# Performance work log

Measured on AMD Instinct MI355X. Metric: run time of the kernel, lower is better.

Reference implementation:

```python
import jax, jax.numpy as jnp
import numpy as np

D_MODEL = 64
SEQ_LEN = 9
MAX_SL = 50
TIMESTAMP = 56
ACTION_NUM = 300
BATCH = 65536


def setup_inputs() -> dict:
    key = jax.random.key(0)
    ks = jax.random.split(key, 8)
    input_actions = jax.random.randint(ks[0], (BATCH, SEQ_LEN), 0, ACTION_NUM + 1)
    emb_table = jax.random.normal(ks[1], (ACTION_NUM + 1, D_MODEL), jnp.float32) * 0.02
    emb_table = emb_table.at[0].set(0.0)  # padding_idx=0
    M_w = jax.random.normal(ks[2], (MAX_SL, D_MODEL, D_MODEL), jnp.float32) * 0.05
    M_b = jax.random.normal(ks[3], (MAX_SL, D_MODEL), jnp.float32) * 0.05
    W_w = jax.random.normal(ks[4], (TIMESTAMP, D_MODEL, D_MODEL), jnp.float32) * 0.05
    W_b = jax.random.normal(ks[5], (TIMESTAMP, D_MODEL), jnp.float32) * 0.05
    out_w = jax.random.normal(ks[6], (ACTION_NUM, D_MODEL), jnp.float32) * 0.05
    out_b = jax.random.normal(ks[7], (ACTION_NUM,), jnp.float32) * 0.05
    return {"input_actions": input_actions, "emb_table": emb_table,
            "M_w": M_w, "M_b": M_b, "W_w": W_w, "W_b": W_b,
            "out_w": out_w, "out_b": out_b}


def reference(input_actions, emb_table, M_w, M_b, W_w, W_b, out_w, out_b):
    B, S = input_actions.shape
    d = emb_table.shape[1]
    ae = emb_table[input_actions]              # [B, S, d]
    ae_t = jnp.transpose(ae, (1, 0, 2))        # [S, B, d]
    # per-timestep weight selection, matching M[min(i, len(M)-1)] and W[i % timeStamp]
    m_idx = jnp.minimum(jnp.arange(S), M_w.shape[0] - 1)
    w_idx = jnp.arange(S) % W_w.shape[0]
    Mw, Mb = M_w[m_idx], M_b[m_idx]            # [S, d, d], [S, d]
    Ww, Wb = W_w[w_idx], W_b[w_idx]

    def step(hl, xs):
        x, mw, mb, ww, wb = xs
        # torch Linear: y = x @ W.T + b
        hl = jax.nn.sigmoid(x @ mw.T + mb + hl @ ww.T + wb)
        return hl, None

    hl0 = jnp.zeros((B, d), ae.dtype)
    hl, _ = jax.lax.scan(step, hl0, (ae_t, Mw, Mb, Ww, Wb))
    return hl @ out_w.T + out_b               # [B, actionNum]
```

## Files before the change

### kernel.cpp

```cpp
#include <hip/hip_runtime.h>
#include <hip/hip_bf16.h>


#define BATCH   65536
#define SEQ     9
#define DMODEL  64
#define ANUM    300
#define BT      64
#define LSTR    72

#define WS_M    0
#define WS_W    36864
#define WS_OW   73728
#define WS_EMB  94208
#define WS_END  113472
#define WS_BSUM_BYTES (WS_END * 2)

typedef __attribute__((ext_vector_type(8))) short  bf16x8;
typedef __attribute__((ext_vector_type(4))) float  f32x4;

__device__ __forceinline__ unsigned short f2b(float f) {
    union { float f; unsigned int u; } x; x.f = f;
    unsigned int r = x.u + 0x7FFFu + ((x.u >> 16) & 1u);
    return (unsigned short)(r >> 16);
}

#define PP_TOTAL (36864 + 20480 + 19264 + 576)

__global__ void prepack(const float* __restrict__ Mw, const float* __restrict__ Ww,
                        const float* __restrict__ outw, const float* __restrict__ emb,
                        const float* __restrict__ Mb, const float* __restrict__ Wb,
                        unsigned short* __restrict__ wsb, float* __restrict__ bsum)
{
    int t = blockIdx.x * 256 + threadIdx.x;
    if (t < 36864) {
        int j    = t & 7;
        int lane = (t >> 3) & 63;
        int kb   = (t >> 9) & 1;
        int nt   = (t >> 10) & 3;
        int s    = t >> 12;
        int nr   = nt * 16 + (lane & 15);
        int k    = kb * 32 + ((lane >> 4) << 3) + j;
        wsb[WS_M + t] = f2b(Mw[(s * DMODEL + nr) * DMODEL + k]);
        wsb[WS_W + t] = f2b(Ww[(s * DMODEL + nr) * DMODEL + k]);
        return;
    }
    t -= 36864;
    if (t < 20480) {
        int j    = t & 7;
        int lane = (t >> 3) & 63;
        int kb   = (t >> 9) & 1;
        int nt   = (t >> 10) & 3;
        int cc   = t >> 12;
        int col  = cc * 64 + nt * 16 + (lane & 15);
        int k    = kb * 32 + ((lane >> 4) << 3) + j;
        float v  = (col < ANUM) ? outw[col * DMODEL + k] : 0.f;
        wsb[WS_OW + t] = f2b(v);
        return;
    }
    t -= 20480;
    if (t < 19264) {
        wsb[WS_EMB + t] = f2b(emb[t]);
        return;
    }
    t -= 19264;
    if (t < 576) {
        bsum[t] = Mb[t] + Wb[t];
    }
}

__global__ __launch_bounds__(256, 4)
void carnn_main(const int* __restrict__ acts,
                const unsigned short* __restrict__ wsb,
                const float* __restrict__ bsum,
                const float* __restrict__ outb,
                float* __restrict__ out)
{
    __shared__ unsigned short Hl[BT * LSTR];

    const int tid  = threadIdx.x;
    const int lane = tid & 63;
    const int wv   = tid >> 6;
    const int lrow = lane & 15;
    const int quad = lane >> 4;
    const int m0   = wv * 16;

    const int brow = blockIdx.x * BT + m0 + lrow;
    const int row9 = brow * SEQ;

    for (int i = lane; i < 16 * LSTR; i += 64) Hl[m0 * LSTR + i] = 0;

    const unsigned short* Mp = wsb + WS_M;
    const unsigned short* Wp = wsb + WS_W;
    const unsigned short* Op = wsb + WS_OW;
    const unsigned short* Eb = wsb + WS_EMB;

    for (int s = 0; s < SEQ; ++s) {
        int id = acts[row9 + s];
        const bf16x8* ex = (const bf16x8*)(Eb + id * DMODEL);
        bf16x8 ax0 = ex[quad];
        bf16x8 ax1 = ex[4 + quad];
        bf16x8 ah0 = *(const bf16x8*)&Hl[(m0 + lrow) * LSTR + quad * 8];
        bf16x8 ah1 = *(const bf16x8*)&Hl[(m0 + lrow) * LSTR + 32 + quad * 8];

        #pragma unroll
        for (int nt = 0; nt < 4; ++nt) {
            const int fo = (s * 4 + nt) * 1024 + lane * 8;
            bf16x8 bm0 = *(const bf16x8*)&Mp[fo];
            bf16x8 bm1 = *(const bf16x8*)&Mp[fo + 512];
            bf16x8 bw0 = *(const bf16x8*)&Wp[fo];
            bf16x8 bw1 = *(const bf16x8*)&Wp[fo + 512];
            f32x4 acc = {0.f, 0.f, 0.f, 0.f};
            acc = __builtin_amdgcn_mfma_f32_16x16x32_bf16(ax0, bm0, acc, 0, 0, 0);
            acc = __builtin_amdgcn_mfma_f32_16x16x32_bf16(ax1, bm1, acc, 0, 0, 0);
            acc = __builtin_amdgcn_mfma_f32_16x16x32_bf16(ah0, bw0, acc, 0, 0, 0);
            acc = __builtin_amdgcn_mfma_f32_16x16x32_bf16(ah1, bw1, acc, 0, 0, 0);

            const int col  = nt * 16 + lrow;
            const float bias = bsum[s * DMODEL + col];
            #pragma unroll
            for (int r = 0; r < 4; ++r) {
                float v = acc[r] + bias;
                float h = 1.f / (1.f + __expf(-v));
                Hl[(m0 + quad * 4 + r) * LSTR + col] = f2b(h);
            }
        }
    }

    bf16x8 ah0 = *(const bf16x8*)&Hl[(m0 + lrow) * LSTR + quad * 8];
    bf16x8 ah1 = *(const bf16x8*)&Hl[(m0 + lrow) * LSTR + 32 + quad * 8];
    const int rowb = blockIdx.x * BT + m0 + quad * 4;

    #pragma unroll
    for (int cc = 0; cc < 5; ++cc) {
        #pragma unroll
        for (int nt = 0; nt < 4; ++nt) {
            const int fo = (cc * 4 + nt) * 1024 + lane * 8;
            bf16x8 b0 = *(const bf16x8*)&Op[fo];
            bf16x8 b1 = *(const bf16x8*)&Op[fo + 512];
            f32x4 acc = {0.f, 0.f, 0.f, 0.f};
            acc = __builtin_amdgcn_mfma_f32_16x16x32_bf16(ah0, b0, acc, 0, 0, 0);
            acc = __builtin_amdgcn_mfma_f32_16x16x32_bf16(ah1, b1, acc, 0, 0, 0);

            const int col = cc * 64 + nt * 16 + lrow;
            if (col < ANUM) {
                const float bias = outb[col];
                #pragma unroll
                for (int r = 0; r < 4; ++r)
                    out[(rowb + r) * ANUM + col] = acc[r] + bias;
            }
        }
    }
}

extern "C" void kernel_launch(void* const* d_in, const int* in_sizes, int n_in,
                              void* d_out, int out_size, void* d_ws, size_t ws_size,
                              hipStream_t stream) {
    const int*   acts = (const int*)  d_in[0];
    const float* emb  = (const float*)d_in[1];
    const float* Mw   = (const float*)d_in[2];
    const float* Mb   = (const float*)d_in[3];
    const float* Ww   = (const float*)d_in[4];
    const float* Wb   = (const float*)d_in[5];
    const float* outw = (const float*)d_in[6];
    const float* outb = (const float*)d_in[7];
    float* out = (float*)d_out;
    (void)in_sizes; (void)n_in; (void)ws_size; (void)out_size;

    unsigned short* wsb = (unsigned short*)d_ws;
    float* bsum = (float*)((char*)d_ws + WS_BSUM_BYTES);

    prepack<<<(PP_TOTAL + 255) / 256, 256, 0, stream>>>(Mw, Ww, outw, emb, Mb, Wb, wsb, bsum);
    carnn_main<<<BATCH / BT, 256, 0, stream>>>(acts, wsb, bsum, outb, out);
}
```

Before: 133.5 us.

## Process two row tiles per wave, prefetch action ids, use fast reciprocal sigmoid

Each wave now handles 32 batch rows as two 16-row tiles, sharing every weight fragment load between two interleaved MFMA chains. All action ids for both tiles are loaded before the recurrence, which removes a dependent global load from each step. The sigmoid uses a hardware reciprocal instead of a divide. Block count halves and launch bounds drop to 2 blocks per CU, trading occupancy for more register-level reuse and ILP.

```diff
diff --git a/kernel.cpp b/kernel.cpp
--- a/kernel.cpp
+++ b/kernel.cpp
@@ -6,7 +6,7 @@
 #define SEQ     9
 #define DMODEL  64
 #define ANUM    300
-#define BT      64
+#define RPB     128
 #define LSTR    72
 
 #define WS_M    0
@@ -23,6 +23,10 @@
     union { float f; unsigned int u; } x; x.f = f;
     unsigned int r = x.u + 0x7FFFu + ((x.u >> 16) & 1u);
     return (unsigned short)(r >> 16);
+}
+
+__device__ __forceinline__ float sigmoid_fast(float v) {
+    return __builtin_amdgcn_rcpf(1.f + __expf(-v));
 }
 
 #define PP_TOTAL (36864 + 20480 + 19264 + 576)
@@ -59,49 +63,58 @@
         return;
     }
     t -= 20480;
-    if (t < 19264) {
-        wsb[WS_EMB + t] = f2b(emb[t]);
-        return;
-    }
+    if (t < 19264) { wsb[WS_EMB + t] = f2b(emb[t]); return; }
     t -= 19264;
-    if (t < 576) {
-        bsum[t] = Mb[t] + Wb[t];
-    }
-}
-
-__global__ __launch_bounds__(256, 4)
+    if (t < 576)   { bsum[t] = Mb[t] + Wb[t]; }
+}
+
+__global__ __launch_bounds__(256, 2)
 void carnn_main(const int* __restrict__ acts,
                 const unsigned short* __restrict__ wsb,
                 const float* __restrict__ bsum,
                 const float* __restrict__ outb,
                 float* __restrict__ out)
 {
-    __shared__ unsigned short Hl[BT * LSTR];
+    __shared__ unsigned short Hl[RPB * LSTR];
 
     const int tid  = threadIdx.x;
     const int lane = tid & 63;
     const int wv   = tid >> 6;
     const int lrow = lane & 15;
     const int quad = lane >> 4;
-    const int m0   = wv * 16;
-
-    const int brow = blockIdx.x * BT + m0 + lrow;
-    const int row9 = brow * SEQ;
-
-    for (int i = lane; i < 16 * LSTR; i += 64) Hl[m0 * LSTR + i] = 0;
+    const int m0   = wv * 32;
+
+    const int bbase = blockIdx.x * RPB;
+
+    for (int i = lane; i < 32 * LSTR; i += 64) Hl[m0 * LSTR + i] = 0;
+
+    const int brow0 = bbase + m0 + lrow;
+    const int brow1 = brow0 + 16;
+    int id0[SEQ], id1[SEQ];
+    #pragma unroll
+    for (int s = 0; s < SEQ; ++s) {
+        id0[s] = acts[brow0 * SEQ + s];
+        id1[s] = acts[brow1 * SEQ + s];
+    }
 
     const unsigned short* Mp = wsb + WS_M;
     const unsigned short* Wp = wsb + WS_W;
     const unsigned short* Op = wsb + WS_OW;
     const unsigned short* Eb = wsb + WS_EMB;
 
+    const int hrow0 = (m0 + lrow) * LSTR;
+    const int hrow1 = (m0 + 16 + lrow) * LSTR;
+
+    #pragma unroll
     for (int s = 0; s < SEQ; ++s) {
-        int id = acts[row9 + s];
-        const bf16x8* ex = (const bf16x8*)(Eb + id * DMODEL);
-        bf16x8 ax0 = ex[quad];
-        bf16x8 ax1 = ex[4 + quad];
-        bf16x8 ah0 = *(const bf16x8*)&Hl[(m0 + lrow) * LSTR + quad * 8];
-        bf16x8 ah1 = *(const bf16x8*)&Hl[(m0 + lrow) * LSTR + 32 + quad * 8];
+        const bf16x8* ex0 = (const bf16x8*)(Eb + id0[s] * DMODEL);
+        const bf16x8* ex1 = (const bf16x8*)(Eb + id1[s] * DMODEL);
+        bf16x8 ax0_0 = ex0[quad],     ax1_0 = ex0[4 + quad];
+        bf16x8 ax0_1 = ex1[quad],     ax1_1 = ex1[4 + quad];
+        bf16x8 ah0_0 = *(const bf16x8*)&Hl[hrow0 + quad * 8];
+        bf16x8 ah1_0 = *(const bf16x8*)&Hl[hrow0 + 32 + quad * 8];
+        bf16x8 ah0_1 = *(const bf16x8*)&Hl[hrow1 + quad * 8];
+        bf16x8 ah1_1 = *(const bf16x8*)&Hl[hrow1 + 32 + quad * 8];
 
         #pragma unroll
         for (int nt = 0; nt < 4; ++nt) {
@@ -110,26 +123,37 @@
             bf16x8 bm1 = *(const bf16x8*)&Mp[fo + 512];
             bf16x8 bw0 = *(const bf16x8*)&Wp[fo];
             bf16x8 bw1 = *(const bf16x8*)&Wp[fo + 512];
-            f32x4 acc = {0.f, 0.f, 0.f, 0.f};
-            acc = __builtin_amdgcn_mfma_f32_16x16x32_bf16(ax0, bm0, acc, 0, 0, 0);
-            acc = __builtin_amdgcn_mfma_f32_16x16x32_bf16(ax1, bm1, acc, 0, 0, 0);
-            acc = __builtin_amdgcn_mfma_f32_16x16x32_bf16(ah0, bw0, acc, 0, 0, 0);
-            acc = __builtin_amdgcn_mfma_f32_16x16x32_bf16(ah1, bw1, acc, 0, 0, 0);
+
+            f32x4 acc0 = {0.f, 0.f, 0.f, 0.f};
+            f32x4 acc1 = {0.f, 0.f, 0.f, 0.f};
+            acc0 = __builtin_amdgcn_mfma_f32_16x16x32_bf16(ax0_0, bm0, acc0, 0, 0, 0);
+            acc1 = __builtin_amdgcn_mfma_f32_16x16x32_bf16(ax0_1, bm0, acc1, 0, 0, 0);
+            acc0 = __builtin_amdgcn_mfma_f32_16x16x32_bf16(ax1_0, bm1, acc0, 0, 0, 0);
+            acc1 = __builtin_amdgcn_mfma_f32_16x16x32_bf16(ax1_1, bm1, acc1, 0, 0, 0);
+            acc0 = __builtin_amdgcn_mfma_f32_16x16x32_bf16(ah0_0, bw0, acc0, 0, 0, 0);
+            acc1 = __builtin_amdgcn_mfma_f32_16x16x32_bf16(ah0_1, bw0, acc1, 0, 0, 0);
+            acc0 = __builtin_amdgcn_mfma_f32_16x16x32_bf16(ah1_0, bw1, acc0, 0, 0, 0);
+            acc1 = __builtin_amdgcn_mfma_f32_16x16x32_bf16(ah1_1, bw1, acc1, 0, 0, 0);
 
             const int col  = nt * 16 + lrow;
             const float bias = bsum[s * DMODEL + col];
+            const int wr0 = (m0 + quad * 4) * LSTR + col;
             #pragma unroll
             for (int r = 0; r < 4; ++r) {
-                float v = acc[r] + bias;
-                float h = 1.f / (1.f + __expf(-v));
-                Hl[(m0 + quad * 4 + r) * LSTR + col] = f2b(h);
+                float h0 = sigmoid_fast(acc0[r] + bias);
+                float h1 = sigmoid_fast(acc1[r] + bias);
+                Hl[wr0 + r * LSTR] = f2b(h0);
+                Hl[wr0 + (16 + r) * LSTR] = f2b(h1);
             }
         }
     }
 
-    bf16x8 ah0 = *(const bf16x8*)&Hl[(m0 + lrow) * LSTR + quad * 8];
-    bf16x8 ah1 = *(const bf16x8*)&Hl[(m0 + lrow) * LSTR + 32 + quad * 8];
-    const int rowb = blockIdx.x * BT + m0 + quad * 4;
+    bf16x8 ah0_0 = *(const bf16x8*)&Hl[hrow0 + quad * 8];
+    bf16x8 ah1_0 = *(const bf16x8*)&Hl[hrow0 + 32 + quad * 8];
+    bf16x8 ah0_1 = *(const bf16x8*)&Hl[hrow1 + quad * 8];
+    bf16x8 ah1_1 = *(const bf16x8*)&Hl[hrow1 + 32 + quad * 8];
+    const int rowb0 = bbase + m0 + quad * 4;
+    const int rowb1 = rowb0 + 16;
 
     #pragma unroll
     for (int cc = 0; cc < 5; ++cc) {
@@ -138,16 +162,21 @@
             const int fo = (cc * 4 + nt) * 1024 + lane * 8;
             bf16x8 b0 = *(const bf16x8*)&Op[fo];
             bf16x8 b1 = *(const bf16x8*)&Op[fo + 512];
-            f32x4 acc = {0.f, 0.f, 0.f, 0.f};
-            acc = __builtin_amdgcn_mfma_f32_16x16x32_bf16(ah0, b0, acc, 0, 0, 0);
-            acc = __builtin_amdgcn_mfma_f32_16x16x32_bf16(ah1, b1, acc, 0, 0, 0);
+            f32x4 acc0 = {0.f, 0.f, 0.f, 0.f};
+            f32x4 acc1 = {0.f, 0.f, 0.f, 0.f};
+            acc0 = __builtin_amdgcn_mfma_f32_16x16x32_bf16(ah0_0, b0, acc0, 0, 0, 0);
+            acc1 = __builtin_amdgcn_mfma_f32_16x16x32_bf16(ah0_1, b0, acc1, 0, 0, 0);
+            acc0 = __builtin_amdgcn_mfma_f32_16x16x32_bf16(ah1_0, b1, acc0, 0, 0, 0);
+            acc1 = __builtin_amdgcn_mfma_f32_16x16x32_bf16(ah1_1, b1, acc1, 0, 0, 0);
 
             const int col = cc * 64 + nt * 16 + lrow;
             if (col < ANUM) {
                 const float bias = outb[col];
                 #pragma unroll
-                for (int r = 0; r < 4; ++r)
-                    out[(rowb + r) * ANUM + col] = acc[r] + bias;
+                for (int r = 0; r < 4; ++r) {
+                    out[(rowb0 + r) * ANUM + col] = acc0[r] + bias;
+                    out[(rowb1 + r) * ANUM + col] = acc1[r] + bias;
+                }
             }
         }
     }
@@ -171,5 +200,5 @@
     float* bsum = (float*)((char*)d_ws + WS_BSUM_BYTES);
 
     prepack<<<(PP_TOTAL + 255) / 256, 256, 0, stream>>>(Mw, Ww, outw, emb, Mb, Wb, wsb, bsum);
-    carnn_main<<<BATCH / BT, 256, 0, stream>>>(acts, wsb, bsum, outb, out);
-}
+    carnn_main<<<BATCH / RPB, 256, 0, stream>>>(acts, wsb, bsum, outb, out);
+}
```

Measured after the change: 149.9 us. 12.3% more time.

## Split each 16-row tile's output columns across two waves with double-buffered hidden state

Applied to the files above, without the earlier changes.

Each block now handles 16 batch rows with two waves, and each wave computes half of the 64 hidden columns per step. The hidden state is double-buffered in LDS with a barrier between steps, so the serial recurrence chain per wave does half the MFMA and sigmoid work. The output projection is likewise split by column tiles. The sigmoid also uses a hardware reciprocal instead of a division. The cost is a block barrier per step, duplicated embedding and hidden loads across the two waves, and four times as many blocks.

```diff
diff --git a/kernel.cpp b/kernel.cpp
--- a/kernel.cpp
+++ b/kernel.cpp
@@ -6,7 +6,6 @@
 #define SEQ     9
 #define DMODEL  64
 #define ANUM    300
-#define BT      64
 #define LSTR    72
 
 #define WS_M    0
@@ -23,6 +22,10 @@
     union { float f; unsigned int u; } x; x.f = f;
     unsigned int r = x.u + 0x7FFFu + ((x.u >> 16) & 1u);
     return (unsigned short)(r >> 16);
+}
+
+__device__ __forceinline__ float sigmoid_fast(float v) {
+    return __builtin_amdgcn_rcpf(1.f + __expf(-v));
 }
 
 #define PP_TOTAL (36864 + 20480 + 19264 + 576)
@@ -59,57 +62,59 @@
         return;
     }
     t -= 20480;
-    if (t < 19264) {
-        wsb[WS_EMB + t] = f2b(emb[t]);
-        return;
-    }
+    if (t < 19264) { wsb[WS_EMB + t] = f2b(emb[t]); return; }
     t -= 19264;
-    if (t < 576) {
-        bsum[t] = Mb[t] + Wb[t];
-    }
+    if (t < 576)   { bsum[t] = Mb[t] + Wb[t]; }
 }
 
-__global__ __launch_bounds__(256, 4)
+__global__ __launch_bounds__(128, 8)
 void carnn_main(const int* __restrict__ acts,
                 const unsigned short* __restrict__ wsb,
                 const float* __restrict__ bsum,
                 const float* __restrict__ outb,
                 float* __restrict__ out)
 {
-    __shared__ unsigned short Hl[BT * LSTR];
+    __shared__ unsigned short Hl[2][16 * LSTR];
 
     const int tid  = threadIdx.x;
     const int lane = tid & 63;
-    const int wv   = tid >> 6;
+    const int w01  = tid >> 6;
     const int lrow = lane & 15;
     const int quad = lane >> 4;
-    const int m0   = wv * 16;
 
-    const int brow = blockIdx.x * BT + m0 + lrow;
-    const int row9 = brow * SEQ;
+    const int brow = blockIdx.x * 16 + lrow;
 
-    for (int i = lane; i < 16 * LSTR; i += 64) Hl[m0 * LSTR + i] = 0;
+    for (int i = tid; i < 16 * LSTR; i += 128) Hl[0][i] = 0;
+    __syncthreads();
 
     const unsigned short* Mp = wsb + WS_M;
     const unsigned short* Wp = wsb + WS_W;
     const unsigned short* Op = wsb + WS_OW;
     const unsigned short* Eb = wsb + WS_EMB;
 
+    const int hoff = lrow * LSTR + quad * 8;
+
+    #pragma unroll
     for (int s = 0; s < SEQ; ++s) {
-        int id = acts[row9 + s];
+        const int rb = s & 1, wb = rb ^ 1;
+
+        bf16x8 ah0 = *(const bf16x8*)&Hl[rb][hoff];
+        bf16x8 ah1 = *(const bf16x8*)&Hl[rb][hoff + 32];
+
+        int id = acts[brow * SEQ + s];
         const bf16x8* ex = (const bf16x8*)(Eb + id * DMODEL);
         bf16x8 ax0 = ex[quad];
         bf16x8 ax1 = ex[4 + quad];
-        bf16x8 ah0 = *(const bf16x8*)&Hl[(m0 + lrow) * LSTR + quad * 8];
-        bf16x8 ah1 = *(const bf16x8*)&Hl[(m0 + lrow) * LSTR + 32 + quad * 8];
 
         #pragma unroll
-        for (int nt = 0; nt < 4; ++nt) {
+        for (int ntl = 0; ntl < 2; ++ntl) {
+            const int nt = w01 * 2 + ntl;
             const int fo = (s * 4 + nt) * 1024 + lane * 8;
             bf16x8 bm0 = *(const bf16x8*)&Mp[fo];
             bf16x8 bm1 = *(const bf16x8*)&Mp[fo + 512];
             bf16x8 bw0 = *(const bf16x8*)&Wp[fo];
             bf16x8 bw1 = *(const bf16x8*)&Wp[fo + 512];
+
             f32x4 acc = {0.f, 0.f, 0.f, 0.f};
             acc = __builtin_amdgcn_mfma_f32_16x16x32_bf16(ax0, bm0, acc, 0, 0, 0);
             acc = __builtin_amdgcn_mfma_f32_16x16x32_bf16(ax1, bm1, acc, 0, 0, 0);
@@ -118,23 +123,25 @@
 
             const int col  = nt * 16 + lrow;
             const float bias = bsum[s * DMODEL + col];
+            const int wr = (quad * 4) * LSTR + col;
             #pragma unroll
             for (int r = 0; r < 4; ++r) {
-                float v = acc[r] + bias;
-                float h = 1.f / (1.f + __expf(-v));
-                Hl[(m0 + quad * 4 + r) * LSTR + col] = f2b(h);
+                float h = sigmoid_fast(acc[r] + bias);
+                Hl[wb][wr + r * LSTR] = f2b(h);
             }
         }
+        __syncthreads();
     }
 
-    bf16x8 ah0 = *(const bf16x8*)&Hl[(m0 + lrow) * LSTR + quad * 8];
-    bf16x8 ah1 = *(const bf16x8*)&Hl[(m0 + lrow) * LSTR + 32 + quad * 8];
-    const int rowb = blockIdx.x * BT + m0 + quad * 4;
+    bf16x8 ah0 = *(const bf16x8*)&Hl[1][hoff];
+    bf16x8 ah1 = *(const bf16x8*)&Hl[1][hoff + 32];
+    const int rowb = blockIdx.x * 16 + quad * 4;
 
     #pragma unroll
     for (int cc = 0; cc < 5; ++cc) {
         #pragma unroll
-        for (int nt = 0; nt < 4; ++nt) {
+        for (int ntl = 0; ntl < 2; ++ntl) {
+            const int nt = w01 * 2 + ntl;
             const int fo = (cc * 4 + nt) * 1024 + lane * 8;
             bf16x8 b0 = *(const bf16x8*)&Op[fo];
             bf16x8 b1 = *(const bf16x8*)&Op[fo + 512];
@@ -171,5 +178,5 @@
     float* bsum = (float*)((char*)d_ws + WS_BSUM_BYTES);
 
     prepack<<<(PP_TOTAL + 255) / 256, 256, 0, stream>>>(Mw, Ww, outw, emb, Mb, Wb, wsb, bsum);
-    carnn_main<<<BATCH / BT, 256, 0, stream>>>(acts, wsb, bsum, outb, out);
+    carnn_main<<<BATCH / 16, 128, 0, stream>>>(acts, wsb, bsum, outb, out);
 }
```

After: 139.4 us. +4.4%, slower.
